# Kernel tuning notes

Hardware: AMD Instinct MI355X
Metric: run time of the kernel (lower is better)

Reference implementation:

```python
import jax, jax.numpy as jnp
import numpy as np

N_DOWN, N_ABOVE, D_IN, D_OUT, FAN_IN = 50000, 100000, 256, 256, 5


def setup_inputs() -> dict:
    key = jax.random.key(0)
    ks = jax.random.split(key, 8)
    h = jax.random.normal(ks[0], (N_DOWN, D_IN), dtype=jnp.float32)
    h_above = jax.random.normal(ks[1], (N_ABOVE, D_IN), dtype=jnp.float32)  # only shape[0] used
    # idx: unique positions of the down nodes within the up-node index space
    idx = jax.random.permutation(ks[2], N_ABOVE)[:N_DOWN]
    # fixed fan-in 5: destination ids i are each node repeated 5 times (DGL bucketing order)
    i = jnp.repeat(jnp.arange(N_ABOVE), FAN_IN)
    j = jax.random.randint(ks[3], (N_ABOVE * FAN_IN,), 0, N_ABOVE)
    s1 = 1.0 / np.sqrt(D_IN * FAN_IN)
    s2 = 1.0 / np.sqrt(D_OUT)
    W1 = jax.random.uniform(ks[4], (D_IN * FAN_IN, D_OUT), jnp.float32, -s1, s1)
    b1 = jax.random.uniform(ks[5], (D_OUT,), jnp.float32, -s1, s1)
    W2 = jax.random.uniform(ks[6], (D_OUT, D_OUT), jnp.float32, -s2, s2)
    b2 = jax.random.uniform(ks[7], (D_OUT,), jnp.float32, -s2, s2)
    return {"h": h, "h_above": h_above, "idx": idx, "i": i, "j": j,
            "W1": W1, "b1": b1, "W2": W2, "b2": b2}


def reference(h, h_above, idx, i, j, W1, b1, W2, b2):
    n_above = h_above.shape[0]
    d = h.shape[1]
    # scatter down-node features into the up-node index space (new_h[idx] = h)
    new_h = jnp.zeros((n_above, d), dtype=h.dtype).at[idx].set(h)
    # gather the 5 source-node messages per destination; i = repeat(arange, 5),
    # so j grouped in blocks of 5 corresponds to each destination's mailbox.
    gathered = new_h[j].reshape(n_above, 5 * d)  # [n_above, 5*d]
    hid = jax.nn.relu(gathered @ W1 + b1)
    return hid @ W2 + b2
```

## Files before the change

### kernel.cpp

```cpp
#include <hip/hip_runtime.h>

#define N_DOWN  50000
#define N_ABOVE 100000
#define DIM     256
#define FAN     5
#define K1      1280
#define MPAD    100096

typedef __bf16 bf16x8 __attribute__((ext_vector_type(8)));
typedef float  f32x4  __attribute__((ext_vector_type(4)));

__device__ __forceinline__ unsigned short f2bf(float f) {
  unsigned u = __builtin_bit_cast(unsigned, f);
  u += 0x7FFFu + ((u >> 16) & 1u);
  return (unsigned short)(u >> 16);
}

__device__ __forceinline__ void gload16(const unsigned short* g, unsigned short* l) {
  __builtin_amdgcn_global_load_lds(
      (const __attribute__((address_space(1))) void*)g,
      (__attribute__((address_space(3))) void*)l, 16, 0, 0);
}

__global__ void k_prep_inv(int* __restrict__ inv, unsigned short* __restrict__ hbf) {
  int t = blockIdx.x * 256 + threadIdx.x;
  if (t < N_ABOVE) inv[t] = N_DOWN;
  if (t < DIM)     hbf[(size_t)N_DOWN * DIM + t] = 0;
}

__device__ __forceinline__ void transpose_tile(const float* __restrict__ in,
                                               unsigned short* __restrict__ out,
                                               int K, int N, int k0, int n0,
                                               float (*tile)[65]) {
  int c = threadIdx.x & 63, rb = threadIdx.x >> 6;
#pragma unroll
  for (int rr = 0; rr < 16; ++rr) {
    int row = rb + rr * 4;
    tile[row][c] = in[(size_t)(k0 + row) * N + n0 + c];
  }
  __syncthreads();
#pragma unroll
  for (int rr = 0; rr < 16; ++rr) {
    int nr = rb + rr * 4;
    out[(size_t)(n0 + nr) * K + k0 + c] = f2bf(tile[c][nr]);
  }
}

__global__ void k_prep_all(const float* __restrict__ h, const int* __restrict__ idx,
                           const float* __restrict__ W1, const float* __restrict__ W2,
                           int* __restrict__ inv, unsigned short* __restrict__ hbf,
                           unsigned short* __restrict__ w1t, unsigned short* __restrict__ w2t) {
  __shared__ float tile[64][65];
  const int b = blockIdx.x;
  if (b < 12500) {
    int t = b * 256 + threadIdx.x;
    float4 v = ((const float4*)h)[t];
    ushort4 o;
    o.x = f2bf(v.x); o.y = f2bf(v.y); o.z = f2bf(v.z); o.w = f2bf(v.w);
    ((ushort4*)hbf)[t] = o;
  } else if (b < 12696) {
    int t = (b - 12500) * 256 + threadIdx.x;
    if (t < N_DOWN) inv[idx[t]] = t;
  } else if (b < 12776) {
    int bb = b - 12696;
    transpose_tile(W1, w1t, K1, DIM, (bb % 20) * 64, (bb / 20) * 64, tile);
  } else {
    int bb = b - 12776;
    transpose_tile(W2, w2t, DIM, DIM, (bb % 4) * 64, (bb / 4) * 64, tile);
  }
}

__global__ __launch_bounds__(256, 2) void k_gemm1(
    const unsigned short* __restrict__ hbf,
    const unsigned short* __restrict__ w1t,
    const float* __restrict__ b1,
    const int* __restrict__ inv,
    const int* __restrict__ jarr,
    unsigned short* __restrict__ hid)
{
  __shared__ __align__(16) unsigned short Alds[128 * 64];
  __shared__ __align__(16) unsigned short Blds[128 * 64];
  __shared__ int srcrow[128 * FAN];

  const int tid = threadIdx.x;
  const int w = tid >> 6, l = tid & 63;
  const int m0 = blockIdx.x * 128, n0 = blockIdx.y * 128;
  const int wm = w >> 1, wn = w & 1;
  const int srow = l >> 3, slot = l & 7;

  for (int e = tid; e < 128 * FAN; e += 256) {
    int row = e / FAN, rr = e - row * FAN;
    int gm = m0 + row;
    int s = N_DOWN;
    if (gm < N_ABOVE) s = inv[jarr[(size_t)gm * FAN + rr]];
    srcrow[e] = s;
  }

  f32x4 acc[4][4] = {};

  for (int t = 0; t < 20; ++t) {
    const int r = t >> 2;
    __syncthreads();
#pragma unroll
    for (int i = 0; i < 4; ++i) {
      int row = w * 32 + i * 8 + srow;
      int src = srcrow[row * FAN + r];
      int c = slot ^ (row & 7);
      gload16(hbf + ((size_t)src << 8) + ((t & 3) << 6) + (c << 3),
              Alds + (w * 32 + i * 8) * 64);
    }
#pragma unroll
    for (int i = 0; i < 4; ++i) {
      int row = w * 32 + i * 8 + srow;
      int c = slot ^ (row & 7);
      gload16(w1t + (size_t)(n0 + row) * K1 + (t << 6) + (c << 3),
              Blds + (w * 32 + i * 8) * 64);
    }
    __syncthreads();

#pragma unroll
    for (int kk = 0; kk < 2; ++kk) {
      bf16x8 af[4], bfr[4];
#pragma unroll
      for (int m = 0; m < 4; ++m) {
        int row = wm * 64 + m * 16 + (l & 15);
        int c = (kk * 4 + (l >> 4)) ^ (row & 7);
        af[m] = *(const bf16x8*)(Alds + row * 64 + c * 8);
      }
#pragma unroll
      for (int n = 0; n < 4; ++n) {
        int row = wn * 64 + n * 16 + (l & 15);
        int c = (kk * 4 + (l >> 4)) ^ (row & 7);
        bfr[n] = *(const bf16x8*)(Blds + row * 64 + c * 8);
      }
#pragma unroll
      for (int m = 0; m < 4; ++m)
#pragma unroll
        for (int n = 0; n < 4; ++n)
          acc[m][n] = __builtin_amdgcn_mfma_f32_16x16x32_bf16(af[m], bfr[n], acc[m][n], 0, 0, 0);
    }
  }

  float bias0 = b1[n0 + wn * 64 + 0 * 16 + (l & 15)];
  float bias1 = b1[n0 + wn * 64 + 1 * 16 + (l & 15)];
  float bias2 = b1[n0 + wn * 64 + 2 * 16 + (l & 15)];
  float bias3 = b1[n0 + wn * 64 + 3 * 16 + (l & 15)];
#pragma unroll
  for (int m = 0; m < 4; ++m) {
#pragma unroll
    for (int q = 0; q < 4; ++q) {
      int gm = m0 + wm * 64 + m * 16 + (l >> 4) * 4 + q;
#pragma unroll
      for (int n = 0; n < 4; ++n) {
        float bias = n == 0 ? bias0 : n == 1 ? bias1 : n == 2 ? bias2 : bias3;
        int gn = n0 + wn * 64 + n * 16 + (l & 15);
        float v = acc[m][n][q] + bias;
        v = v > 0.f ? v : 0.f;
        hid[(size_t)gm * DIM + gn] = f2bf(v);
      }
    }
  }
}

__global__ __launch_bounds__(512, 2) void k_gemm2(
    const unsigned short* __restrict__ hid,
    const unsigned short* __restrict__ w2t,
    const float* __restrict__ b2,
    float* __restrict__ out)
{
  __shared__ __align__(16) unsigned short Alds[128 * 64];
  __shared__ __align__(16) unsigned short Blds[256 * 64];

  const int tid = threadIdx.x;
  const int w = tid >> 6, l = tid & 63;
  const int m0 = blockIdx.x * 128;
  const int wm = w >> 2, wn = w & 3;
  const int srow = l >> 3, slot = l & 7;

  f32x4 acc[4][4] = {};

  for (int t = 0; t < 4; ++t) {
    __syncthreads();
#pragma unroll
    for (int i = 0; i < 2; ++i) {
      int row = w * 16 + i * 8 + srow;
      int c = slot ^ (row & 7);
      gload16(hid + (size_t)(m0 + row) * DIM + (t << 6) + (c << 3),
              Alds + (w * 16 + i * 8) * 64);
    }
#pragma unroll
    for (int i = 0; i < 4; ++i) {
      int row = w * 32 + i * 8 + srow;
      int c = slot ^ (row & 7);
      gload16(w2t + (size_t)row * DIM + (t << 6) + (c << 3),
              Blds + (w * 32 + i * 8) * 64);
    }
    __syncthreads();

#pragma unroll
    for (int kk = 0; kk < 2; ++kk) {
      bf16x8 af[4], bfr[4];
#pragma unroll
      for (int m = 0; m < 4; ++m) {
        int row = wm * 64 + m * 16 + (l & 15);
        int c = (kk * 4 + (l >> 4)) ^ (row & 7);
        af[m] = *(const bf16x8*)(Alds + row * 64 + c * 8);
      }
#pragma unroll
      for (int n = 0; n < 4; ++n) {
        int row = wn * 64 + n * 16 + (l & 15);
        int c = (kk * 4 + (l >> 4)) ^ (row & 7);
        bfr[n] = *(const bf16x8*)(Blds + row * 64 + c * 8);
      }
#pragma unroll
      for (int m = 0; m < 4; ++m)
#pragma unroll
        for (int n = 0; n < 4; ++n)
          acc[m][n] = __builtin_amdgcn_mfma_f32_16x16x32_bf16(af[m], bfr[n], acc[m][n], 0, 0, 0);
    }
  }

  float bias0 = b2[wn * 64 + 0 * 16 + (l & 15)];
  float bias1 = b2[wn * 64 + 1 * 16 + (l & 15)];
  float bias2 = b2[wn * 64 + 2 * 16 + (l & 15)];
  float bias3 = b2[wn * 64 + 3 * 16 + (l & 15)];
#pragma unroll
  for (int m = 0; m < 4; ++m) {
#pragma unroll
    for (int q = 0; q < 4; ++q) {
      int gm = m0 + wm * 64 + m * 16 + (l >> 4) * 4 + q;
      if (gm < N_ABOVE) {
#pragma unroll
        for (int n = 0; n < 4; ++n) {
          float bias = n == 0 ? bias0 : n == 1 ? bias1 : n == 2 ? bias2 : bias3;
          int gn = wn * 64 + n * 16 + (l & 15);
          out[(size_t)gm * DIM + gn] = acc[m][n][q] + bias;
        }
      }
    }
  }
}

extern "C" void kernel_launch(void* const* d_in, const int* in_sizes, int n_in,
                              void* d_out, int out_size, void* d_ws, size_t ws_size,
                              hipStream_t stream) {
  const float* h    = (const float*)d_in[0];
  const int*   idx  = (const int*)d_in[2];
  const int*   jarr = (const int*)d_in[4];
  const float* W1   = (const float*)d_in[5];
  const float* b1   = (const float*)d_in[6];
  const float* W2   = (const float*)d_in[7];
  const float* b2   = (const float*)d_in[8];
  float* out = (float*)d_out;

  char* ws = (char*)d_ws;
  size_t off = 0;
  auto alloc = [&](size_t bytes) -> void* {
    void* p = ws + off;
    off += bytes;
    off = (off + 511) & ~(size_t)511;
    return p;
  };
  int*            inv = (int*)alloc((size_t)N_ABOVE * 4);
  unsigned short* hbf = (unsigned short*)alloc((size_t)(N_DOWN + 1) * DIM * 2);
  unsigned short* w1t = (unsigned short*)alloc((size_t)DIM * K1 * 2);
  unsigned short* w2t = (unsigned short*)alloc((size_t)DIM * DIM * 2);
  unsigned short* hid = (unsigned short*)alloc((size_t)MPAD * DIM * 2);
  if (ws_size < off) return;

  k_prep_inv<<<dim3(391), dim3(256), 0, stream>>>(inv, hbf);
  k_prep_all<<<dim3(12792), dim3(256), 0, stream>>>(h, idx, W1, W2, inv, hbf, w1t, w2t);
  k_gemm1<<<dim3(MPAD / 128, 2), dim3(256), 0, stream>>>(hbf, w1t, b1, inv, jarr, hid);
  k_gemm2<<<dim3(MPAD / 128), dim3(512), 0, stream>>>(hid, w2t, b2, out);
}
```

Before: 124.4 us.

## Widen gemm1 tile to full N=256 and replace prep_inv kernel with memsets

Result: slower. 128.2 us (+3.1%).

```diff
diff --git a/kernel.cpp b/kernel.cpp
--- a/kernel.cpp
+++ b/kernel.cpp
@@ -20,12 +20,6 @@
   __builtin_amdgcn_global_load_lds(
       (const __attribute__((address_space(1))) void*)g,
       (__attribute__((address_space(3))) void*)l, 16, 0, 0);
-}
-
-__global__ void k_prep_inv(int* __restrict__ inv, unsigned short* __restrict__ hbf) {
-  int t = blockIdx.x * 256 + threadIdx.x;
-  if (t < N_ABOVE) inv[t] = N_DOWN;
-  if (t < DIM)     hbf[(size_t)N_DOWN * DIM + t] = 0;
 }
 
 __device__ __forceinline__ void transpose_tile(const float* __restrict__ in,
@@ -70,7 +64,7 @@
   }
 }
 
-__global__ __launch_bounds__(256, 2) void k_gemm1(
+__global__ __launch_bounds__(512, 2) void k_gemm1(
     const unsigned short* __restrict__ hbf,
     const unsigned short* __restrict__ w1t,
     const float* __restrict__ b1,
@@ -79,21 +73,24 @@
     unsigned short* __restrict__ hid)
 {
   __shared__ __align__(16) unsigned short Alds[128 * 64];
-  __shared__ __align__(16) unsigned short Blds[128 * 64];
-  __shared__ int srcrow[128 * FAN];
+  __shared__ __align__(16) unsigned short Blds[256 * 64];
+  __shared__ unsigned short srcrow[128 * FAN];
 
   const int tid = threadIdx.x;
   const int w = tid >> 6, l = tid & 63;
-  const int m0 = blockIdx.x * 128, n0 = blockIdx.y * 128;
-  const int wm = w >> 1, wn = w & 1;
+  const int m0 = blockIdx.x * 128;
+  const int wm = w >> 2, wn = w & 3;
   const int srow = l >> 3, slot = l & 7;
 
-  for (int e = tid; e < 128 * FAN; e += 256) {
+  for (int e = tid; e < 128 * FAN; e += 512) {
     int row = e / FAN, rr = e - row * FAN;
     int gm = m0 + row;
     int s = N_DOWN;
-    if (gm < N_ABOVE) s = inv[jarr[(size_t)gm * FAN + rr]];
-    srcrow[e] = s;
+    if (gm < N_ABOVE) {
+      s = inv[jarr[(size_t)gm * FAN + rr]];
+      if (s < 0) s = N_DOWN;
+    }
+    srcrow[e] = (unsigned short)s;
   }
 
   f32x4 acc[4][4] = {};
@@ -102,18 +99,18 @@
     const int r = t >> 2;
     __syncthreads();
 #pragma unroll
+    for (int i = 0; i < 2; ++i) {
+      int row = w * 16 + i * 8 + srow;
+      int src = srcrow[row * FAN + r];
+      int c = slot ^ (row & 7);
+      gload16(hbf + ((size_t)src << 8) + ((t & 3) << 6) + (c << 3),
+              Alds + (w * 16 + i * 8) * 64);
+    }
+#pragma unroll
     for (int i = 0; i < 4; ++i) {
       int row = w * 32 + i * 8 + srow;
-      int src = srcrow[row * FAN + r];
-      int c = slot ^ (row & 7);
-      gload16(hbf + ((size_t)src << 8) + ((t & 3) << 6) + (c << 3),
-              Alds + (w * 32 + i * 8) * 64);
-    }
-#pragma unroll
-    for (int i = 0; i < 4; ++i) {
-      int row = w * 32 + i * 8 + srow;
-      int c = slot ^ (row & 7);
-      gload16(w1t + (size_t)(n0 + row) * K1 + (t << 6) + (c << 3),
+      int c = slot ^ (row & 7);
+      gload16(w1t + (size_t)row * K1 + (t << 6) + (c << 3),
               Blds + (w * 32 + i * 8) * 64);
     }
     __syncthreads();
@@ -141,10 +138,10 @@
     }
   }
 
-  float bias0 = b1[n0 + wn * 64 + 0 * 16 + (l & 15)];
-  float bias1 = b1[n0 + wn * 64 + 1 * 16 + (l & 15)];
-  float bias2 = b1[n0 + wn * 64 + 2 * 16 + (l & 15)];
-  float bias3 = b1[n0 + wn * 64 + 3 * 16 + (l & 15)];
+  float bias0 = b1[wn * 64 + 0 * 16 + (l & 15)];
+  float bias1 = b1[wn * 64 + 1 * 16 + (l & 15)];
+  float bias2 = b1[wn * 64 + 2 * 16 + (l & 15)];
+  float bias3 = b1[wn * 64 + 3 * 16 + (l & 15)];
 #pragma unroll
   for (int m = 0; m < 4; ++m) {
 #pragma unroll
@@ -153,7 +150,7 @@
 #pragma unroll
       for (int n = 0; n < 4; ++n) {
         float bias = n == 0 ? bias0 : n == 1 ? bias1 : n == 2 ? bias2 : bias3;
-        int gn = n0 + wn * 64 + n * 16 + (l & 15);
+        int gn = wn * 64 + n * 16 + (l & 15);
         float v = acc[m][n][q] + bias;
         v = v > 0.f ? v : 0.f;
         hid[(size_t)gm * DIM + gn] = f2bf(v);
@@ -268,8 +265,9 @@
   unsigned short* hid = (unsigned short*)alloc((size_t)MPAD * DIM * 2);
   if (ws_size < off) return;
 
-  k_prep_inv<<<dim3(391), dim3(256), 0, stream>>>(inv, hbf);
+  hipMemsetAsync(inv, 0xFF, (size_t)N_ABOVE * 4, stream);
+  hipMemsetAsync(hbf + (size_t)N_DOWN * DIM, 0, DIM * 2, stream);
   k_prep_all<<<dim3(12792), dim3(256), 0, stream>>>(h, idx, W1, W2, inv, hbf, w1t, w2t);
-  k_gemm1<<<dim3(MPAD / 128, 2), dim3(256), 0, stream>>>(hbf, w1t, b1, inv, jarr, hid);
+  k_gemm1<<<dim3(MPAD / 128), dim3(512), 0, stream>>>(hbf, w1t, b1, inv, jarr, hid);
   k_gemm2<<<dim3(MPAD / 128), dim3(512), 0, stream>>>(hid, w2t, b2, out);
 }
```
